# Optimization experiments

Hardware: AMD Instinct MI355X
Metric: run time of the kernel (lower is better)

The kernel has to match this reference:

```python
import jax, jax.numpy as jnp
import numpy as np

N_SPK = 2048   # number of speakers
U = 32         # utterances per speaker (half enrollment, half test)
D = 256        # embedding dim
EPS = 1e-8     # F.cosine_similarity eps (norm clamp)


def setup_inputs() -> dict:
    key = jax.random.key(0)
    k1, = jax.random.split(key, 1)
    embeddings = jax.random.normal(k1, (N_SPK * U, D), dtype=jnp.float32)
    labels = jnp.repeat(jnp.arange(N_SPK, dtype=jnp.int64), U)
    alpha = jnp.float32(10.0)
    beta = jnp.float32(-5.0)
    return {"embeddings": embeddings, "labels": labels, "alpha": alpha, "beta": beta}


def _ge2e_loss(embeddings, labels_np, alpha, beta):
    # labels_np: host numpy int labels (constant). Balanced: each speaker has U utts.
    n_spk = int(labels_np.max()) + 1
    u = labels_np.shape[0] // n_spk
    order = np.argsort(labels_np, kind="stable")  # group by speaker, preserve order
    emb = embeddings[order].reshape(n_spk, u, -1)           # [N, U, D]
    half = u // 2
    enroll, test = emb[:, :half], emb[:, half:]             # [N, U/2, D]
    cent = enroll.mean(axis=1)                              # [N, D]
    tn = test / jnp.maximum(jnp.linalg.norm(test, axis=-1, keepdims=True), EPS)
    cn = cent / jnp.maximum(jnp.linalg.norm(cent, axis=-1, keepdims=True), EPS)
    # cosine sim of every test utt (speaker m, utt t) vs every centroid n
    sims = alpha * jnp.einsum("mtd,nd->mtn", tn, cn) + beta  # [N, U/2, N]
    e = jnp.exp(sims)
    total = e.sum(axis=(0, 1))                               # [N] sum over all test utts per centroid
    idx = jnp.arange(n_spk)
    pos_sum = e[idx, :, idx].sum(axis=1)                     # [N] own-speaker test utts
    neg_sum = total - pos_sum                                # sum over other speakers' test utts
    loss = jnp.mean(jnp.log(neg_sum) - jnp.log(pos_sum))
    return loss


def reference(embeddings, labels, alpha, beta):
    labels_np = np.asarray(labels)
    return _ge2e_loss(embeddings, labels_np, alpha, beta)
```

## Files before the change

### kernel.cpp

```cpp
#include <hip/hip_runtime.h>
#include <hip/hip_bf16.h>
#include <stdint.h>

#define N_SPK 2048
#define UU 32
#define DD 256
#define HALF_U 16
#define M_ROWS (N_SPK * HALF_U)

#define BM 128
#define BN 128
#define BK 64

typedef __attribute__((ext_vector_type(8))) short short8;
typedef __attribute__((ext_vector_type(4))) float f32x4;

typedef const __attribute__((address_space(1))) void ga_void;
typedef __attribute__((address_space(3))) void ls_void;

__device__ __forceinline__ void gld16(const void* g, void* l) {
    __builtin_amdgcn_global_load_lds((ga_void*)(uintptr_t)g,
                                     (ls_void*)(uintptr_t)l, 16, 0, 0);
}

__device__ __forceinline__ unsigned short f2bf(float x) {
    union { float f; unsigned u; } c; c.f = x;
    unsigned r = c.u + 0x7fffu + ((c.u >> 16) & 1u);
    return (unsigned short)(r >> 16);
}

__global__ __launch_bounds__(256) void prep_kernel(const float* __restrict__ emb,
                                                   unsigned short* __restrict__ tn,
                                                   unsigned short* __restrict__ cn)
{
    const int w = threadIdx.x >> 6;
    const int l = threadIdx.x & 63;
    const int task = blockIdx.x * 4 + w;

    float4 v;
    if (task < M_ROWS) {
        const int m = task >> 4;
        const int t = task & 15;
        const size_t grow = (size_t)m * UU + HALF_U + t;
        v = *(const float4*)(emb + grow * DD + 4 * l);
    } else {
        const int n = task - M_ROWS;
        float ax = 0.f, ay = 0.f, az = 0.f, aw = 0.f;
        const float* base = emb + (size_t)n * UU * DD + 4 * l;
        #pragma unroll
        for (int j = 0; j < HALF_U; ++j) {
            float4 e = *(const float4*)(base + j * DD);
            ax += e.x; ay += e.y; az += e.z; aw += e.w;
        }
        const float inv = 1.0f / 16.0f;
        v = make_float4(ax * inv, ay * inv, az * inv, aw * inv);
    }
    float ss = v.x * v.x + v.y * v.y + v.z * v.z + v.w * v.w;
    #pragma unroll
    for (int d = 1; d < 64; d <<= 1) ss += __shfl_xor(ss, d);
    const float sc = 1.0f / fmaxf(sqrtf(ss), 1e-8f);

    ushort4 o;
    o.x = f2bf(v.x * sc); o.y = f2bf(v.y * sc);
    o.z = f2bf(v.z * sc); o.w = f2bf(v.w * sc);
    unsigned short* dst = (task < M_ROWS)
        ? (tn + (size_t)task * DD + 4 * l)
        : (cn + (size_t)(task - M_ROWS) * DD + 4 * l);
    *(ushort4*)dst = o;
}

__device__ __forceinline__ void stage_tiles(const char* gA, const char* gB,
                                            char* ldsA, char* ldsB,
                                            int k0b, int w, int l)
{
    #pragma unroll
    for (int i = 0; i < 4; ++i) {
        const int off = (w * 4 + i) * 1024 + l * 16;
        const int row = off >> 7;
        const int sc  = ((off >> 4) & 7) ^ (row & 7);
        const int goff = row * 512 + k0b + sc * 16;
        gld16(gA + goff, ldsA + off);
        gld16(gB + goff, ldsB + off);
    }
}

__device__ __forceinline__ void compute_step(const char* Asb, const char* Bsb,
                                             f32x4 (&acc)[4][4],
                                             int wr, int wc, int r16, int hi)
{
    #pragma unroll
    for (int kk = 0; kk < 2; ++kk) {
        short8 a[4], b[4];
        #pragma unroll
        for (int mi = 0; mi < 4; ++mi) {
            const int row = wr * 64 + mi * 16 + r16;
            const int c16 = (kk * 4 + hi) ^ (row & 7);
            a[mi] = *(const short8*)(Asb + row * 128 + c16 * 16);
        }
        #pragma unroll
        for (int ni = 0; ni < 4; ++ni) {
            const int row = wc * 64 + ni * 16 + r16;
            const int c16 = (kk * 4 + hi) ^ (row & 7);
            b[ni] = *(const short8*)(Bsb + row * 128 + c16 * 16);
        }
        #pragma unroll
        for (int mi = 0; mi < 4; ++mi)
            #pragma unroll
            for (int ni = 0; ni < 4; ++ni)
                acc[mi][ni] = __builtin_amdgcn_mfma_f32_16x16x32_bf16(
                    a[mi], b[ni], acc[mi][ni], 0, 0, 0);
    }
}

__global__ __launch_bounds__(256) void gemm_kernel(const unsigned short* __restrict__ tnb,
                                                   const unsigned short* __restrict__ cnb,
                                                   const float* __restrict__ alphaP,
                                                   const float* __restrict__ betaP,
                                                   float* __restrict__ total,
                                                   float* __restrict__ pos)
{
    __shared__ __align__(16) char As[2][BM * BK * 2];
    __shared__ __align__(16) char Bs[2][BN * BK * 2];
    __shared__ float colsum[BN];

    const int tid = threadIdx.x;
    const int l = tid & 63;
    const int w = tid >> 6;
    const int wr = w >> 1, wc = w & 1;
    const int r16 = l & 15, hi = l >> 4;
    const int bn = blockIdx.x;
    const int bm = blockIdx.y;

    const char* gA = (const char*)tnb + (size_t)bm * BM * 512;
    const char* gB = (const char*)cnb + (size_t)bn * BN * 512;

    f32x4 acc[4][4] = {};

    stage_tiles(gA, gB, As[0], Bs[0], 0, w, l);
    if (tid < BN) colsum[tid] = 0.0f;
    __syncthreads();

    int buf = 0;
    #pragma unroll
    for (int kt = 0; kt < 4; ++kt) {
        if (kt < 3) stage_tiles(gA, gB, As[buf ^ 1], Bs[buf ^ 1], (kt + 1) * BK * 2, w, l);
        compute_step(As[buf], Bs[buf], acc, wr, wc, r16, hi);
        __syncthreads();
        buf ^= 1;
    }

    const float alpha = *alphaP;
    const float beta  = *betaP;

    #pragma unroll
    for (int ni = 0; ni < 4; ++ni) {
        const int colg = bn * BN + wc * 64 + ni * 16 + r16;
        float csum = 0.f;
        #pragma unroll
        for (int mi = 0; mi < 4; ++mi) {
            const int rowbase = bm * BM + wr * 64 + mi * 16 + hi * 4;
            #pragma unroll
            for (int r = 0; r < 4; ++r) {
                const float e = __expf(alpha * acc[mi][ni][r] + beta);
                csum += e;
                if (((rowbase + r) >> 4) == colg)
                    atomicAdd(pos + colg, e);
            }
        }
        csum += __shfl_xor(csum, 16);
        csum += __shfl_xor(csum, 32);
        if (hi == 0) atomicAdd(&colsum[wc * 64 + ni * 16 + r16], csum);
    }
    __syncthreads();
    if (tid < BN) atomicAdd(total + bn * BN + tid, colsum[tid]);
}

__global__ __launch_bounds__(256) void finalize_kernel(const float* __restrict__ total,
                                                       const float* __restrict__ pos,
                                                       float* __restrict__ out)
{
    const int tid = threadIdx.x;
    float s = 0.f;
    for (int i = tid; i < N_SPK; i += 256) {
        const float p = pos[i];
        const float t = total[i];
        s += logf(t - p) - logf(p);
    }
    #pragma unroll
    for (int d = 1; d < 64; d <<= 1) s += __shfl_xor(s, d);
    __shared__ float wsum[4];
    if ((tid & 63) == 0) wsum[tid >> 6] = s;
    __syncthreads();
    if (tid == 0) out[0] = (wsum[0] + wsum[1] + wsum[2] + wsum[3]) * (1.0f / (float)N_SPK);
}

extern "C" void kernel_launch(void* const* d_in, const int* in_sizes, int n_in,
                              void* d_out, int out_size, void* d_ws, size_t ws_size,
                              hipStream_t stream)
{
    const float* emb    = (const float*)d_in[0];
    const float* alphaP = (const float*)d_in[2];
    const float* betaP  = (const float*)d_in[3];
    float* out = (float*)d_out;

    char* ws = (char*)d_ws;
    unsigned short* tn = (unsigned short*)ws;
    unsigned short* cn = (unsigned short*)(ws + 16777216);
    float* total       = (float*)(ws + 16777216 + 1048576);
    float* pos         = total + N_SPK;

    hipMemsetAsync(total, 0, 2 * N_SPK * sizeof(float), stream);

    hipLaunchKernelGGL(prep_kernel, dim3((M_ROWS + N_SPK) / 4), dim3(256), 0, stream,
                       emb, tn, cn);
    hipLaunchKernelGGL(gemm_kernel, dim3(N_SPK / BN, M_ROWS / BM), dim3(256), 0, stream,
                       tn, cn, alphaP, betaP, total, pos);
    hipLaunchKernelGGL(finalize_kernel, dim3(1), dim3(256), 0, stream,
                       total, pos, out);
}
```

Baseline: 170.1 us.

## Enlarge GEMM tiles to 256x256 with 512 threads and explicit prefetch pipeline

Doubles the GEMM block tile to 256x256 with 8 waves, each wave computing 128x64, so every tile loaded from global memory is reused more. The K loop is unrolled by hand with two stages in flight, using explicit vmcnt waits and raw barriers in place of __syncthreads. Blocks are remapped so consecutive block IDs share B tiles, and colsum reuses the A LDS buffer. Costs are more LDS (128KB), one block per CU, higher register pressure, and fewer blocks in the grid.

```diff
diff --git a/kernel.cpp b/kernel.cpp
--- a/kernel.cpp
+++ b/kernel.cpp
@@ -8,8 +8,8 @@
 #define HALF_U 16
 #define M_ROWS (N_SPK * HALF_U)
 
-#define BM 128
-#define BN 128
+#define BM 256
+#define BN 256
 #define BK 64
 
 typedef __attribute__((ext_vector_type(8))) short short8;
@@ -69,34 +69,27 @@
     *(ushort4*)dst = o;
 }
 
-__device__ __forceinline__ void stage_tiles(const char* gA, const char* gB,
-                                            char* ldsA, char* ldsB,
-                                            int k0b, int w, int l)
+__device__ __forceinline__ void stage_kt(const char* gA, const char* gB,
+                                         char* lA, char* lB, int ktb, int tid)
 {
     #pragma unroll
     for (int i = 0; i < 4; ++i) {
-        const int off = (w * 4 + i) * 1024 + l * 16;
+        const int off = i * 8192 + tid * 16;
         const int row = off >> 7;
         const int sc  = ((off >> 4) & 7) ^ (row & 7);
-        const int goff = row * 512 + k0b + sc * 16;
-        gld16(gA + goff, ldsA + off);
-        gld16(gB + goff, ldsB + off);
-    }
-}
-
-__device__ __forceinline__ void compute_step(const char* Asb, const char* Bsb,
-                                             f32x4 (&acc)[4][4],
-                                             int wr, int wc, int r16, int hi)
+        const int goff = row * 512 + ktb + sc * 16;
+        gld16(gA + goff, lA + off);
+        gld16(gB + goff, lB + off);
+    }
+}
+
+__device__ __forceinline__ void compute_kt(const char* Asb, const char* Bsb,
+                                           f32x4 (&acc)[8][4],
+                                           int wr, int wc, int r16, int hi)
 {
     #pragma unroll
     for (int kk = 0; kk < 2; ++kk) {
-        short8 a[4], b[4];
-        #pragma unroll
-        for (int mi = 0; mi < 4; ++mi) {
-            const int row = wr * 64 + mi * 16 + r16;
-            const int c16 = (kk * 4 + hi) ^ (row & 7);
-            a[mi] = *(const short8*)(Asb + row * 128 + c16 * 16);
-        }
+        short8 b[4];
         #pragma unroll
         for (int ni = 0; ni < 4; ++ni) {
             const int row = wc * 64 + ni * 16 + r16;
@@ -104,50 +97,76 @@
             b[ni] = *(const short8*)(Bsb + row * 128 + c16 * 16);
         }
         #pragma unroll
-        for (int mi = 0; mi < 4; ++mi)
+        for (int mi = 0; mi < 8; ++mi) {
+            const int row = wr * 128 + mi * 16 + r16;
+            const int c16 = (kk * 4 + hi) ^ (row & 7);
+            const short8 a = *(const short8*)(Asb + row * 128 + c16 * 16);
             #pragma unroll
             for (int ni = 0; ni < 4; ++ni)
                 acc[mi][ni] = __builtin_amdgcn_mfma_f32_16x16x32_bf16(
-                    a[mi], b[ni], acc[mi][ni], 0, 0, 0);
-    }
-}
-
-__global__ __launch_bounds__(256) void gemm_kernel(const unsigned short* __restrict__ tnb,
-                                                   const unsigned short* __restrict__ cnb,
-                                                   const float* __restrict__ alphaP,
-                                                   const float* __restrict__ betaP,
-                                                   float* __restrict__ total,
-                                                   float* __restrict__ pos)
+                    a, b[ni], acc[mi][ni], 0, 0, 0);
+        }
+    }
+}
+
+#define WAITVM(n) do { \
+    asm volatile("s_waitcnt vmcnt(" #n ")" ::: "memory"); \
+    __builtin_amdgcn_sched_barrier(0); \
+} while (0)
+
+__global__ __launch_bounds__(512, 1) void gemm_kernel(const unsigned short* __restrict__ tnb,
+                                                      const unsigned short* __restrict__ cnb,
+                                                      const float* __restrict__ alphaP,
+                                                      const float* __restrict__ betaP,
+                                                      float* __restrict__ total,
+                                                      float* __restrict__ pos)
 {
     __shared__ __align__(16) char As[2][BM * BK * 2];
     __shared__ __align__(16) char Bs[2][BN * BK * 2];
-    __shared__ float colsum[BN];
 
     const int tid = threadIdx.x;
     const int l = tid & 63;
     const int w = tid >> 6;
-    const int wr = w >> 1, wc = w & 1;
+    const int wr = w >> 2, wc = w & 3;
     const int r16 = l & 15, hi = l >> 4;
-    const int bn = blockIdx.x;
-    const int bm = blockIdx.y;
+
+    const int bid = blockIdx.x;
+    const int tile = (bid & 7) * 128 + (bid >> 3);
+    const int bm = tile >> 3;
+    const int bn = tile & 7;
 
     const char* gA = (const char*)tnb + (size_t)bm * BM * 512;
     const char* gB = (const char*)cnb + (size_t)bn * BN * 512;
 
-    f32x4 acc[4][4] = {};
-
-    stage_tiles(gA, gB, As[0], Bs[0], 0, w, l);
+    f32x4 acc[8][4] = {};
+
+    stage_kt(gA, gB, As[0], Bs[0], 0 * 128, tid);
+    stage_kt(gA, gB, As[1], Bs[1], 1 * 128, tid);
+    WAITVM(8);
+    __builtin_amdgcn_s_barrier();
+
+    compute_kt(As[0], Bs[0], acc, wr, wc, r16, hi);
+    __builtin_amdgcn_s_barrier();
+    stage_kt(gA, gB, As[0], Bs[0], 2 * 128, tid);
+    WAITVM(8);
+    __builtin_amdgcn_s_barrier();
+
+    compute_kt(As[1], Bs[1], acc, wr, wc, r16, hi);
+    __builtin_amdgcn_s_barrier();
+    stage_kt(gA, gB, As[1], Bs[1], 3 * 128, tid);
+    WAITVM(8);
+    __builtin_amdgcn_s_barrier();
+
+    compute_kt(As[0], Bs[0], acc, wr, wc, r16, hi);
+    WAITVM(0);
+    __builtin_amdgcn_s_barrier();
+
+    compute_kt(As[1], Bs[1], acc, wr, wc, r16, hi);
+
+    __builtin_amdgcn_s_barrier();
+    float* colsum = (float*)As;
     if (tid < BN) colsum[tid] = 0.0f;
-    __syncthreads();
-
-    int buf = 0;
-    #pragma unroll
-    for (int kt = 0; kt < 4; ++kt) {
-        if (kt < 3) stage_tiles(gA, gB, As[buf ^ 1], Bs[buf ^ 1], (kt + 1) * BK * 2, w, l);
-        compute_step(As[buf], Bs[buf], acc, wr, wc, r16, hi);
-        __syncthreads();
-        buf ^= 1;
-    }
+    __builtin_amdgcn_s_barrier();
 
     const float alpha = *alphaP;
     const float beta  = *betaP;
@@ -157,8 +176,8 @@
         const int colg = bn * BN + wc * 64 + ni * 16 + r16;
         float csum = 0.f;
         #pragma unroll
-        for (int mi = 0; mi < 4; ++mi) {
-            const int rowbase = bm * BM + wr * 64 + mi * 16 + hi * 4;
+        for (int mi = 0; mi < 8; ++mi) {
+            const int rowbase = bm * BM + wr * 128 + mi * 16 + hi * 4;
             #pragma unroll
             for (int r = 0; r < 4; ++r) {
                 const float e = __expf(alpha * acc[mi][ni][r] + beta);
@@ -213,7 +232,7 @@
 
     hipLaunchKernelGGL(prep_kernel, dim3((M_ROWS + N_SPK) / 4), dim3(256), 0, stream,
                        emb, tn, cn);
-    hipLaunchKernelGGL(gemm_kernel, dim3(N_SPK / BN, M_ROWS / BM), dim3(256), 0, stream,
+    hipLaunchKernelGGL(gemm_kernel, dim3(M_ROWS / BM * (N_SPK / BN)), dim3(512), 0, stream,
                        tn, cn, alphaP, betaP, total, pos);
     hipLaunchKernelGGL(finalize_kernel, dim3(1), dim3(256), 0, stream,
                        total, pos, out);
```

Result: faster. 159.5 us (-6.3%).

## Single-buffer GEMM tiles, remap blocks across XCDs, fold memset into prep

Applied to the files above, without the earlier changes.

Switches the GEMM from double-buffered LDS staging to a single buffer with load-sync-compute-sync per K step, halving LDS use so launch_bounds can request three blocks per CU. It uses a 1D grid with a tile remap that spreads consecutive block IDs across eight groups, for locality on multi-die parts. It also skips the diagonal test on non-diagonal tiles and zeroes the accumulators inside prep_kernel instead of a separate memset. The price is that global-to-LDS loads no longer overlap with MFMA work inside a block, so latency hiding now depends on having more resident blocks.

```diff
diff --git a/kernel.cpp b/kernel.cpp
--- a/kernel.cpp
+++ b/kernel.cpp
@@ -31,8 +31,14 @@
 
 __global__ __launch_bounds__(256) void prep_kernel(const float* __restrict__ emb,
                                                    unsigned short* __restrict__ tn,
-                                                   unsigned short* __restrict__ cn)
-{
+                                                   unsigned short* __restrict__ cn,
+                                                   float* __restrict__ zbuf)
+{
+    if (blockIdx.x == 0) {
+        #pragma unroll
+        for (int i = 0; i < 16; ++i) zbuf[threadIdx.x + 256 * i] = 0.0f;
+    }
+
     const int w = threadIdx.x >> 6;
     const int l = threadIdx.x & 63;
     const int task = blockIdx.x * 4 + w;
@@ -69,110 +75,98 @@
     *(ushort4*)dst = o;
 }
 
-__device__ __forceinline__ void stage_tiles(const char* gA, const char* gB,
-                                            char* ldsA, char* ldsB,
-                                            int k0b, int w, int l)
-{
-    #pragma unroll
-    for (int i = 0; i < 4; ++i) {
-        const int off = (w * 4 + i) * 1024 + l * 16;
-        const int row = off >> 7;
-        const int sc  = ((off >> 4) & 7) ^ (row & 7);
-        const int goff = row * 512 + k0b + sc * 16;
-        gld16(gA + goff, ldsA + off);
-        gld16(gB + goff, ldsB + off);
-    }
-}
-
-__device__ __forceinline__ void compute_step(const char* Asb, const char* Bsb,
-                                             f32x4 (&acc)[4][4],
-                                             int wr, int wc, int r16, int hi)
-{
-    #pragma unroll
-    for (int kk = 0; kk < 2; ++kk) {
-        short8 a[4], b[4];
-        #pragma unroll
-        for (int mi = 0; mi < 4; ++mi) {
-            const int row = wr * 64 + mi * 16 + r16;
-            const int c16 = (kk * 4 + hi) ^ (row & 7);
-            a[mi] = *(const short8*)(Asb + row * 128 + c16 * 16);
-        }
-        #pragma unroll
-        for (int ni = 0; ni < 4; ++ni) {
-            const int row = wc * 64 + ni * 16 + r16;
-            const int c16 = (kk * 4 + hi) ^ (row & 7);
-            b[ni] = *(const short8*)(Bsb + row * 128 + c16 * 16);
-        }
-        #pragma unroll
-        for (int mi = 0; mi < 4; ++mi)
-            #pragma unroll
-            for (int ni = 0; ni < 4; ++ni)
-                acc[mi][ni] = __builtin_amdgcn_mfma_f32_16x16x32_bf16(
-                    a[mi], b[ni], acc[mi][ni], 0, 0, 0);
-    }
-}
-
-__global__ __launch_bounds__(256) void gemm_kernel(const unsigned short* __restrict__ tnb,
-                                                   const unsigned short* __restrict__ cnb,
-                                                   const float* __restrict__ alphaP,
-                                                   const float* __restrict__ betaP,
-                                                   float* __restrict__ total,
-                                                   float* __restrict__ pos)
-{
-    __shared__ __align__(16) char As[2][BM * BK * 2];
-    __shared__ __align__(16) char Bs[2][BN * BK * 2];
-    __shared__ float colsum[BN];
+__global__ __launch_bounds__(256, 3) void gemm_kernel(const unsigned short* __restrict__ tnb,
+                                                      const unsigned short* __restrict__ cnb,
+                                                      const float* __restrict__ alphaP,
+                                                      const float* __restrict__ betaP,
+                                                      float* __restrict__ total,
+                                                      float* __restrict__ pos)
+{
+    __shared__ __align__(16) char As[BM * BK * 2];
+    __shared__ __align__(16) char Bs[BN * BK * 2];
+    __shared__ float csum[BN];
 
     const int tid = threadIdx.x;
     const int l = tid & 63;
     const int w = tid >> 6;
     const int wr = w >> 1, wc = w & 1;
     const int r16 = l & 15, hi = l >> 4;
-    const int bn = blockIdx.x;
-    const int bm = blockIdx.y;
+
+    const int bid = blockIdx.x;
+    const int tile = (bid & 7) * 512 + (bid >> 3);
+    const int bm = tile >> 4;
+    const int bn = tile & 15;
 
     const char* gA = (const char*)tnb + (size_t)bm * BM * 512;
     const char* gB = (const char*)cnb + (size_t)bn * BN * 512;
 
     f32x4 acc[4][4] = {};
 
-    stage_tiles(gA, gB, As[0], Bs[0], 0, w, l);
-    if (tid < BN) colsum[tid] = 0.0f;
-    __syncthreads();
-
-    int buf = 0;
-    #pragma unroll
     for (int kt = 0; kt < 4; ++kt) {
-        if (kt < 3) stage_tiles(gA, gB, As[buf ^ 1], Bs[buf ^ 1], (kt + 1) * BK * 2, w, l);
-        compute_step(As[buf], Bs[buf], acc, wr, wc, r16, hi);
+        #pragma unroll
+        for (int i = 0; i < 4; ++i) {
+            const int off = i * 4096 + tid * 16;
+            const int row = off >> 7;
+            const int sc  = ((off >> 4) & 7) ^ (row & 7);
+            const int goff = row * 512 + kt * 128 + sc * 16;
+            gld16(gA + goff, As + off);
+            gld16(gB + goff, Bs + off);
+        }
         __syncthreads();
-        buf ^= 1;
+
+        #pragma unroll
+        for (int kk = 0; kk < 2; ++kk) {
+            short8 a[4], b[4];
+            #pragma unroll
+            for (int ni = 0; ni < 4; ++ni) {
+                const int row = wc * 64 + ni * 16 + r16;
+                const int c16 = (kk * 4 + hi) ^ (row & 7);
+                b[ni] = *(const short8*)(Bs + row * 128 + c16 * 16);
+            }
+            #pragma unroll
+            for (int mi = 0; mi < 4; ++mi) {
+                const int row = wr * 64 + mi * 16 + r16;
+                const int c16 = (kk * 4 + hi) ^ (row & 7);
+                a[mi] = *(const short8*)(As + row * 128 + c16 * 16);
+            }
+            #pragma unroll
+            for (int mi = 0; mi < 4; ++mi)
+                #pragma unroll
+                for (int ni = 0; ni < 4; ++ni)
+                    acc[mi][ni] = __builtin_amdgcn_mfma_f32_16x16x32_bf16(
+                        a[mi], b[ni], acc[mi][ni], 0, 0, 0);
+        }
+        __syncthreads();
     }
 
     const float alpha = *alphaP;
     const float beta  = *betaP;
+    const bool diag = ((bm >> 4) == bn);
+
+    if (tid < BN) csum[tid] = 0.0f;
+    __syncthreads();
 
     #pragma unroll
     for (int ni = 0; ni < 4; ++ni) {
         const int colg = bn * BN + wc * 64 + ni * 16 + r16;
-        float csum = 0.f;
+        float cs = 0.f;
         #pragma unroll
         for (int mi = 0; mi < 4; ++mi) {
             const int rowbase = bm * BM + wr * 64 + mi * 16 + hi * 4;
             #pragma unroll
             for (int r = 0; r < 4; ++r) {
                 const float e = __expf(alpha * acc[mi][ni][r] + beta);
-                csum += e;
-                if (((rowbase + r) >> 4) == colg)
+                cs += e;
+                if (diag && ((rowbase + r) >> 4) == colg)
                     atomicAdd(pos + colg, e);
             }
         }
-        csum += __shfl_xor(csum, 16);
-        csum += __shfl_xor(csum, 32);
-        if (hi == 0) atomicAdd(&colsum[wc * 64 + ni * 16 + r16], csum);
+        cs += __shfl_xor(cs, 16);
+        cs += __shfl_xor(cs, 32);
+        if (hi == 0) atomicAdd(&csum[wc * 64 + ni * 16 + r16], cs);
     }
     __syncthreads();
-    if (tid < BN) atomicAdd(total + bn * BN + tid, colsum[tid]);
+    if (tid < BN) atomicAdd(total + bn * BN + tid, csum[tid]);
 }
 
 __global__ __launch_bounds__(256) void finalize_kernel(const float* __restrict__ total,
@@ -209,11 +203,9 @@
     float* total       = (float*)(ws + 16777216 + 1048576);
     float* pos         = total + N_SPK;
 
-    hipMemsetAsync(total, 0, 2 * N_SPK * sizeof(float), stream);
-
     hipLaunchKernelGGL(prep_kernel, dim3((M_ROWS + N_SPK) / 4), dim3(256), 0, stream,
-                       emb, tn, cn);
-    hipLaunchKernelGGL(gemm_kernel, dim3(N_SPK / BN, M_ROWS / BM), dim3(256), 0, stream,
+                       emb, tn, cn, total );
+    hipLaunchKernelGGL(gemm_kernel, dim3(M_ROWS / BM * (N_SPK / BN)), dim3(256), 0, stream,
                        tn, cn, alphaP, betaP, total, pos);
     hipLaunchKernelGGL(finalize_kernel, dim3(1), dim3(256), 0, stream,
                        total, pos, out);
```

Result: faster. 153.7 us (-9.7%).
